# Kernel tuning notes

Hardware: AMD Instinct MI355X
Metric: run time of the kernel (lower is better)

Reference implementation:

```python
import jax, jax.numpy as jnp
import numpy as np

HEAD_NUM = 8
NEG = 10000.0


def setup_inputs() -> dict:
    key = jax.random.key(0)
    ks = jax.random.split(key, 8)
    B, S, D = 2, 2048, 512
    sc = 1.0 / np.sqrt(D)
    return {
        "x": jax.random.normal(ks[0], (B, S, D), dtype=jnp.float32),
        "mask": jax.random.randint(ks[1], (B, S), 0, 2, dtype=jnp.int32),
        "Wq": jax.random.normal(ks[2], (D, D), dtype=jnp.float32) * sc,
        "bq": jnp.zeros((D,), jnp.float32),
        "Wk": jax.random.normal(ks[3], (D, D), dtype=jnp.float32) * sc,
        "bk": jnp.zeros((D,), jnp.float32),
        "Wv": jax.random.normal(ks[4], (D, D), dtype=jnp.float32) * sc,
        "bv": jnp.zeros((D,), jnp.float32),
        "Wo": jax.random.normal(ks[5], (D, D), dtype=jnp.float32) * sc,
        "bo": jnp.zeros((D,), jnp.float32),
    }


def _split_heads(t, H):
    B, S, D = t.shape
    return t.reshape(B, S, H, D // H).transpose(0, 2, 1, 3)  # [B,H,S,hd]


def reference(x, mask, Wq, bq, Wk, bk, Wv, bv, Wo, bo):
    B, S, D = x.shape
    H = HEAD_NUM
    hd = D // H
    # linear projections + relu activation (as in keras layer)
    q = jax.nn.relu(x @ Wq + bq)
    k = jax.nn.relu(x @ Wk + bk)
    v = jax.nn.relu(x @ Wv + bv)
    q = _split_heads(q, H)
    k = _split_heads(k, H)
    v = _split_heads(v, H)
    # scaled dot-product scores: scale by sqrt(head_dim) (query last dim after split)
    e = jnp.einsum("bhqd,bhkd->bhqk", q, k) / jnp.sqrt(jnp.float32(hd))
    # causal (history_only) additive mask
    idx = jnp.arange(S)
    causal = (idx[None, :] > idx[:, None]).astype(jnp.float32)  # [S,S]
    e = e - NEG * causal[None, None, :, :]
    # key padding mask, additive
    e = e - NEG * (1.0 - mask.astype(jnp.float32))[:, None, None, :]
    # stable softmax (explicit max-subtract as in source)
    a = jax.nn.softmax(e, axis=-1)
    out = jnp.einsum("bhqk,bhkd->bhqd", a, v)  # [B,H,S,hd]
    out = out.transpose(0, 2, 1, 3).reshape(B, S, D)
    # output projection + activation
    return jax.nn.relu(out @ Wo + bo)
```

## Files before the change

### kernel.cpp

```cpp
#include <hip/hip_runtime.h>
#include <hip/hip_bf16.h>

constexpr int Bc = 2, Sc = 2048, Dc = 512, Hc = 8, HDc = 64;
constexpr int Mtot = Bc * Sc;
constexpr size_t HEADMAT = (size_t)Bc * Hc * Sc * HDc;
constexpr float SC2  = 0.18033688011112042f;
constexpr float NEG2 = 14426.950408889634f;

typedef __attribute__((ext_vector_type(8)))  short          short8;
typedef __attribute__((ext_vector_type(8)))  unsigned short ushort8;
typedef __attribute__((ext_vector_type(4)))  float          f32x4;
typedef __attribute__((ext_vector_type(16))) float          f32x16;

#define MFMA16 __builtin_amdgcn_mfma_f32_16x16x32_bf16
#define MFMA32 __builtin_amdgcn_mfma_f32_32x32x16_bf16

static __device__ __forceinline__ unsigned short f32_to_bf16_bits(float f) {
    unsigned int u = __builtin_bit_cast(unsigned int, f);
    unsigned int r = u + 0x7FFFu + ((u >> 16) & 1u);
    return (unsigned short)(r >> 16);
}
static __device__ __forceinline__ unsigned int pkbf(float a, float b) {
    return (unsigned int)f32_to_bf16_bits(a) |
           ((unsigned int)f32_to_bf16_bits(b) << 16);
}

__global__ __launch_bounds__(256)
void convert_x(const float* __restrict__ x, unsigned short* __restrict__ Xb, int n)
{
    const int i = (blockIdx.x * 256 + threadIdx.x) * 4;
    if (i >= n) return;
    const float4 v = *(const float4*)(x + i);
    ushort4 o;
    o.x = f32_to_bf16_bits(v.x);
    o.y = f32_to_bf16_bits(v.y);
    o.z = f32_to_bf16_bits(v.z);
    o.w = f32_to_bf16_bits(v.w);
    *(ushort4*)(Xb + i) = o;
}

__global__ __launch_bounds__(256)
void transpose_w(const float* __restrict__ W0, const float* __restrict__ W1,
                 const float* __restrict__ W2, const float* __restrict__ W3,
                 unsigned short* __restrict__ Wt)
{
    __shared__ float T[64][65];
    const int z = blockIdx.z;
    const float* Wp = (z == 0) ? W0 : (z == 1) ? W1 : (z == 2) ? W2 : W3;
    unsigned short* Op = Wt + (size_t)z * 512 * 512;

    const int kt = blockIdx.y * 64, nt = blockIdx.x * 64;
    const int t = threadIdx.x;
    const int r  = t >> 2, c4 = (t & 3) * 16;

    #pragma unroll
    for (int i = 0; i < 4; ++i) {
        const float4 v = *(const float4*)(Wp + (size_t)(kt + r) * 512 + nt + c4 + 4 * i);
        T[r][c4 + 4*i + 0] = v.x;
        T[r][c4 + 4*i + 1] = v.y;
        T[r][c4 + 4*i + 2] = v.z;
        T[r][c4 + 4*i + 3] = v.w;
    }
    __syncthreads();

    const int n = t >> 2, k4 = (t & 3) * 16;
    #pragma unroll
    for (int i = 0; i < 4; ++i) {
        ushort4 o;
        o.x = f32_to_bf16_bits(T[k4 + 4*i + 0][n]);
        o.y = f32_to_bf16_bits(T[k4 + 4*i + 1][n]);
        o.z = f32_to_bf16_bits(T[k4 + 4*i + 2][n]);
        o.w = f32_to_bf16_bits(T[k4 + 4*i + 3][n]);
        *(ushort4*)(Op + (size_t)(nt + n) * 512 + kt + k4 + 4 * i) = o;
    }
}

template<bool HEADOUT>
__global__ __launch_bounds__(256)
void gemm_tile(const unsigned short* __restrict__ Xb,
               const unsigned short* __restrict__ Wt,
               const float* __restrict__ b0, const float* __restrict__ b1,
               const float* __restrict__ b2,
               unsigned short* __restrict__ Hout,
               float* __restrict__ Yf)
{
    __shared__ short As[128 * 32];
    __shared__ short Bs[64 * 32];

    const int lane = threadIdx.x & 63, wave = threadIdx.x >> 6;
    const int c = lane & 15, g = lane >> 4;
    const int wr = wave >> 1, wc = wave & 1;
    const int z = blockIdx.z;
    const unsigned short* Wp = Wt + (size_t)z * 512 * 512;
    const float* bp = (z == 0) ? b0 : (z == 1) ? b1 : b2;
    const int bm = blockIdx.y * 128;
    const int bn = blockIdx.x * 64;

    const int srow = lane >> 2;
    const int scol = (lane & 3) * 8;

    f32x4 acc[4][2] = {};

    for (int k0 = 0; k0 < 512; k0 += 32) {
        __syncthreads();
        #pragma unroll
        for (int i = 0; i < 2; ++i) {
            const int row = (wave * 2 + i) * 16 + srow;
            const short8 v = *(const short8*)(Xb + (size_t)(bm + row) * 512 + k0 + scol);
            *(short8*)(&As[row * 32 + scol]) = v;
        }
        {
            const int row = wave * 16 + srow;
            const short8 v = *(const short8*)(Wp + (size_t)(bn + row) * 512 + k0 + scol);
            *(short8*)(&Bs[row * 32 + scol]) = v;
        }
        __syncthreads();

        short8 a[4], bfr[2];
        #pragma unroll
        for (int mi = 0; mi < 4; ++mi)
            a[mi] = *(const short8*)(&As[(wr * 64 + mi * 16 + c) * 32 + g * 8]);
        #pragma unroll
        for (int ni = 0; ni < 2; ++ni)
            bfr[ni] = *(const short8*)(&Bs[(wc * 32 + ni * 16 + c) * 32 + g * 8]);
        #pragma unroll
        for (int mi = 0; mi < 4; ++mi)
            #pragma unroll
            for (int ni = 0; ni < 2; ++ni)
                acc[mi][ni] = MFMA16(a[mi], bfr[ni], acc[mi][ni], 0, 0, 0);
    }

    #pragma unroll
    for (int mi = 0; mi < 4; ++mi) {
        #pragma unroll
        for (int ni = 0; ni < 2; ++ni) {
            const int n = bn + wc * 32 + ni * 16 + c;
            const float bias = bp[n];
            float v[4];
            #pragma unroll
            for (int r = 0; r < 4; ++r)
                v[r] = fmaxf(acc[mi][ni][r] + bias, 0.0f);
            const int mbase = bm + wr * 64 + mi * 16 + 4 * g;
            if constexpr (HEADOUT) {
                const int bb = mbase >> 11, ss = mbase & 2047;
                const int hh = n >> 6, hd = n & 63;
                if (z == 2) {
                    union { ushort4 u; unsigned short s[4]; } pk;
                    #pragma unroll
                    for (int r = 0; r < 4; ++r) pk.s[r] = f32_to_bf16_bits(v[r]);
                    *reinterpret_cast<ushort4*>(
                        Hout + (size_t)2 * HEADMAT +
                        ((size_t)(bb * Hc + hh) * HDc + hd) * Sc + ss) = pk.u;
                } else {
                    #pragma unroll
                    for (int r = 0; r < 4; ++r)
                        Hout[(size_t)z * HEADMAT +
                             (((size_t)(bb * Hc + hh) * Sc + ss + r) * HDc + hd)] =
                            f32_to_bf16_bits(v[r]);
                }
            } else {
                #pragma unroll
                for (int r = 0; r < 4; ++r)
                    Yf[(size_t)(mbase + r) * 512 + n] = v[r];
            }
        }
    }
}

__global__ __launch_bounds__(256)
void attn_mfma(const short* __restrict__ Qh, const short* __restrict__ Kh,
               const short* __restrict__ Vt, const int* __restrict__ mask,
               unsigned short* __restrict__ Ob)
{
    __shared__ __align__(16) char smem[4 * 8448 + 4 * 256];

    const int lane = threadIdx.x & 63;
    const int wave = threadIdx.x >> 6;
    const int bid  = blockIdx.x;
    const int swz  = (bid & 7) * 128 + (bid >> 3);
    const int t    = swz & 63;
    const int h    = (swz >> 6) & 7;
    const int b    = swz >> 9;
    const int q0   = t * 32;
    const int r32  = lane & 31;
    const int hi   = lane >> 5;

    char*  wreg = smem + wave * 8448;
    float* Lml  = (float*)(smem + 4 * 8448 + wave * 256);

    const size_t headoff = (size_t)(b * Hc + h) * Sc * HDc;
    const short* Qp = Qh + headoff;
    const short* Kp = Kh + headoff;
    const short* Vp = Vt + headoff;
    const int* mb = mask + b * Sc;

    int fb = Sc;
    for (int base = 0; base < Sc; base += 64) {
        unsigned long long bal = __ballot(mb[base + lane] != 0);
        if (bal) { fb = base + (__ffsll(bal) - 1); break; }
    }
    const int kmax = (fb <= q0) ? (q0 + 32) : Sc;
    const int kend = (kmax + 31) & ~31;
    const int nT   = kend >> 5;
    const int tpw  = (nT + 3) >> 2;
    const int kbeg = wave * tpw * 32;
    const int kfin = min(kend, kbeg + tpw * 32);

    short8 qf[4];
    #pragma unroll
    for (int j = 0; j < 4; ++j)
        qf[j] = *(const short8*)(Qp + (size_t)(q0 + r32) * HDc + j * 16 + hi * 8);

    f32x16 acc0 = {0,0,0,0,0,0,0,0,0,0,0,0,0,0,0,0};
    f32x16 acc1 = {0,0,0,0,0,0,0,0,0,0,0,0,0,0,0,0};
    float m = -1e30f, l = 0.0f;

    const short* vrow0 = Vp + (size_t)r32 * Sc + 8 * hi;
    const short* vrow1 = Vp + (size_t)(32 + r32) * Sc + 8 * hi;

    for (int k0 = kbeg; k0 < kfin; k0 += 32) {
        const short8 va0 = *(const short8*)(vrow0 + k0);
        const short8 va1 = *(const short8*)(vrow0 + k0 + 16);
        const short8 vb0 = *(const short8*)(vrow1 + k0);
        const short8 vb1 = *(const short8*)(vrow1 + k0 + 16);

        f32x16 s = {0,0,0,0,0,0,0,0,0,0,0,0,0,0,0,0};
        #pragma unroll
        for (int j = 0; j < 4; ++j) {
            const short8 kf =
                *(const short8*)(Kp + (size_t)(k0 + r32) * HDc + j * 16 + hi * 8);
            s = MFMA32(kf, qf[j], s, 0, 0, 0);
        }

        const unsigned long long bal = __ballot(mb[k0 + r32] != 0);
        const unsigned int mloc = ((unsigned int)bal) >> (4 * hi);

        float e[16];
        float tmax = -1e30f;
        if (k0 + 31 > q0) {
            #pragma unroll
            for (int r = 0; r < 16; ++r) {
                const int cr0 = (r & 3) + 8 * (r >> 2);
                float ev = s[r] * SC2;
                if (!((mloc >> cr0) & 1))            ev -= NEG2;
                if (k0 + cr0 + 4 * hi > q0 + r32)    ev -= NEG2;
                e[r] = ev;
                tmax = fmaxf(tmax, ev);
            }
        } else {
            #pragma unroll
            for (int r = 0; r < 16; ++r) {
                const int cr0 = (r & 3) + 8 * (r >> 2);
                float ev = s[r] * SC2;
                if (!((mloc >> cr0) & 1))            ev -= NEG2;
                e[r] = ev;
                tmax = fmaxf(tmax, ev);
            }
        }
        tmax = fmaxf(tmax, __shfl_xor(tmax, 32));

        if (__any(tmax > m)) {
            const float mn   = fmaxf(m, tmax);
            const float corr = __builtin_exp2f(m - mn);
            m = mn; l *= corr;
            acc0 *= corr;
            acc1 *= corr;
        }

        float ps = 0.f;
        #pragma unroll
        for (int r = 0; r < 16; ++r) {
            e[r] = __builtin_exp2f(e[r] - m);
            ps += e[r];
        }
        l += ps;

        const unsigned int A0 = pkbf(e[0],  e[1]),  B0 = pkbf(e[2],  e[3]);
        const unsigned int C0 = pkbf(e[4],  e[5]),  D0 = pkbf(e[6],  e[7]);
        const unsigned int A1 = pkbf(e[8],  e[9]),  B1 = pkbf(e[10], e[11]);
        const unsigned int C1 = pkbf(e[12], e[13]), D1 = pkbf(e[14], e[15]);
        const unsigned int A0s = (unsigned int)__shfl_xor((int)A0, 32);
        const unsigned int B0s = (unsigned int)__shfl_xor((int)B0, 32);
        const unsigned int C0s = (unsigned int)__shfl_xor((int)C0, 32);
        const unsigned int D0s = (unsigned int)__shfl_xor((int)D0, 32);
        const unsigned int A1s = (unsigned int)__shfl_xor((int)A1, 32);
        const unsigned int B1s = (unsigned int)__shfl_xor((int)B1, 32);
        const unsigned int C1s = (unsigned int)__shfl_xor((int)C1, 32);
        const unsigned int D1s = (unsigned int)__shfl_xor((int)D1, 32);

        union { unsigned int u[4]; short8 s8; } P0, P1;
        P0.u[0] = hi ? C0s : A0;  P0.u[1] = hi ? D0s : B0;
        P0.u[2] = hi ? C0  : A0s; P0.u[3] = hi ? D0  : B0s;
        P1.u[0] = hi ? C1s : A1;  P1.u[1] = hi ? D1s : B1;
        P1.u[2] = hi ? C1  : A1s; P1.u[3] = hi ? D1  : B1s;

        acc0 = MFMA32(va0, P0.s8, acc0, 0, 0, 0);
        acc0 = MFMA32(va1, P1.s8, acc0, 0, 0, 0);
        acc1 = MFMA32(vb0, P0.s8, acc1, 0, 0, 0);
        acc1 = MFMA32(vb1, P1.s8, acc1, 0, 0, 0);
    }

    l += __shfl_xor(l, 32);

    {
        float* Lacc = (float*)wreg;
        #pragma unroll
        for (int r = 0; r < 16; ++r) {
            Lacc[lane * 33 + r]      = acc0[r];
            Lacc[lane * 33 + 16 + r] = acc1[r];
        }
        if (lane < 32) { Lml[lane] = m; Lml[32 + lane] = l; }
    }
    __syncthreads();

    float mu[4], lu[4], M = -1e30f;
    #pragma unroll
    for (int u = 0; u < 4; ++u) {
        const float* LmlU = (const float*)(smem + 4 * 8448 + u * 256);
        mu[u] = LmlU[r32];
        lu[u] = LmlU[32 + r32];
        M = fmaxf(M, mu[u]);
    }
    float wgt[4], L = 0.f;
    #pragma unroll
    for (int u = 0; u < 4; ++u) {
        wgt[u] = __builtin_exp2f(mu[u] - M);
        L += wgt[u] * lu[u];
    }
    const float invL = 1.0f / L;

    #pragma unroll
    for (int jj = 0; jj < 8; ++jj) {
        const int j = wave * 8 + jj;
        float o = 0.f;
        #pragma unroll
        for (int u = 0; u < 4; ++u)
            o += wgt[u] * ((const float*)(smem + u * 8448))[lane * 33 + j];
        const int j16 = j & 15;
        const int d = (j16 & 3) + 8 * (j16 >> 2) + 4 * hi + 32 * (j >> 4);
        Ob[(size_t)(b * Sc + q0 + r32) * Dc + h * HDc + d] =
            f32_to_bf16_bits(o * invL);
    }
}

extern "C" void kernel_launch(void* const* d_in, const int* in_sizes, int n_in,
                              void* d_out, int out_size, void* d_ws, size_t ws_size,
                              hipStream_t stream) {
    const float* x  = (const float*)d_in[0];
    const int* mask = (const int*)d_in[1];
    const float* Wq = (const float*)d_in[2];
    const float* bq = (const float*)d_in[3];
    const float* Wk = (const float*)d_in[4];
    const float* bk = (const float*)d_in[5];
    const float* Wv = (const float*)d_in[6];
    const float* bv = (const float*)d_in[7];
    const float* Wo = (const float*)d_in[8];
    const float* bo = (const float*)d_in[9];
    float* out = (float*)d_out;

    unsigned short* Xb = (unsigned short*)d_ws;
    unsigned short* Wt = Xb + (size_t)Mtot * 512;
    unsigned short* Qh = Wt + (size_t)4 * 512 * 512;
    unsigned short* Kh = Qh + HEADMAT;
    unsigned short* Vt = Kh + HEADMAT;
    unsigned short* Ob = Vt + HEADMAT;

    convert_x<<<dim3((Mtot * 512) / 1024), dim3(256), 0, stream>>>(
        x, Xb, Mtot * 512);
    transpose_w<<<dim3(8, 8, 4), dim3(256), 0, stream>>>(Wq, Wk, Wv, Wo, Wt);
    gemm_tile<true><<<dim3(8, Mtot / 128, 3), dim3(256), 0, stream>>>(
        Xb, Wt, bq, bk, bv, Qh, nullptr);
    attn_mfma<<<dim3(1024), dim3(256), 0, stream>>>(
        (const short*)Qh, (const short*)Kh, (const short*)Vt, mask, Ob);
    gemm_tile<false><<<dim3(8, Mtot / 128, 1), dim3(256), 0, stream>>>(
        Ob, Wt + (size_t)3 * 512 * 512, bo, bo, bo, nullptr, out);
}
```

Measured before the change: 97.49 us.

## Split attention key range across eight waves and fold softmax scale into Q

Launches the attention kernel with 512 threads so eight waves each process a share of the key range, then merges partial accumulators in two rounds through the same shared-memory buffer. The softmax scale is folded into the Q projection epilogue, which removes a multiply per score. The bf16 packing now uses the HIP intrinsic, and the tile order is reversed so the long causal tiles launch first. Extra block barriers and the merge step add overhead, and scaling Q before bf16 rounding slightly changes the numerics.

```diff
diff --git a/kernel.cpp b/kernel.cpp
--- a/kernel.cpp
+++ b/kernel.cpp
@@ -20,9 +20,10 @@
     unsigned int r = u + 0x7FFFu + ((u >> 16) & 1u);
     return (unsigned short)(r >> 16);
 }
-static __device__ __forceinline__ unsigned int pkbf(float a, float b) {
-    return (unsigned int)f32_to_bf16_bits(a) |
-           ((unsigned int)f32_to_bf16_bits(b) << 16);
+static __device__ __forceinline__ unsigned int pk2bf(float a, float b) {
+    union { __hip_bfloat162 h2; unsigned int u; } cv;
+    cv.h2 = __float22bfloat162_rn(make_float2(a, b));
+    return cv.u;
 }
 
 __global__ __launch_bounds__(256)
@@ -138,8 +139,10 @@
             const float bias = bp[n];
             float v[4];
             #pragma unroll
-            for (int r = 0; r < 4; ++r)
+            for (int r = 0; r < 4; ++r) {
                 v[r] = fmaxf(acc[mi][ni][r] + bias, 0.0f);
+                if (HEADOUT && z == 0) v[r] *= SC2;
+            }
             const int mbase = bm + wr * 64 + mi * 16 + 4 * g;
             if constexpr (HEADOUT) {
                 const int bb = mbase >> 11, ss = mbase & 2047;
@@ -167,26 +170,25 @@
     }
 }
 
-__global__ __launch_bounds__(256)
+__global__ __launch_bounds__(512, 4)
 void attn_mfma(const short* __restrict__ Qh, const short* __restrict__ Kh,
                const short* __restrict__ Vt, const int* __restrict__ mask,
                unsigned short* __restrict__ Ob)
 {
-    __shared__ __align__(16) char smem[4 * 8448 + 4 * 256];
+    __shared__ __align__(16) char smem[4 * 8448 + 8 * 256];
 
     const int lane = threadIdx.x & 63;
     const int wave = threadIdx.x >> 6;
     const int bid  = blockIdx.x;
     const int swz  = (bid & 7) * 128 + (bid >> 3);
-    const int t    = swz & 63;
+    const int t    = 63 - (swz & 63);
     const int h    = (swz >> 6) & 7;
     const int b    = swz >> 9;
     const int q0   = t * 32;
     const int r32  = lane & 31;
     const int hi   = lane >> 5;
 
-    char*  wreg = smem + wave * 8448;
-    float* Lml  = (float*)(smem + 4 * 8448 + wave * 256);
+    float* Lml = (float*)(smem + 4 * 8448 + wave * 256);
 
     const size_t headoff = (size_t)(b * Hc + h) * Sc * HDc;
     const short* Qp = Qh + headoff;
@@ -202,7 +204,7 @@
     const int kmax = (fb <= q0) ? (q0 + 32) : Sc;
     const int kend = (kmax + 31) & ~31;
     const int nT   = kend >> 5;
-    const int tpw  = (nT + 3) >> 2;
+    const int tpw  = (nT + 7) >> 3;
     const int kbeg = wave * tpw * 32;
     const int kfin = min(kend, kbeg + tpw * 32);
 
@@ -241,7 +243,7 @@
             #pragma unroll
             for (int r = 0; r < 16; ++r) {
                 const int cr0 = (r & 3) + 8 * (r >> 2);
-                float ev = s[r] * SC2;
+                float ev = s[r];
                 if (!((mloc >> cr0) & 1))            ev -= NEG2;
                 if (k0 + cr0 + 4 * hi > q0 + r32)    ev -= NEG2;
                 e[r] = ev;
@@ -251,7 +253,7 @@
             #pragma unroll
             for (int r = 0; r < 16; ++r) {
                 const int cr0 = (r & 3) + 8 * (r >> 2);
-                float ev = s[r] * SC2;
+                float ev = s[r];
                 if (!((mloc >> cr0) & 1))            ev -= NEG2;
                 e[r] = ev;
                 tmax = fmaxf(tmax, ev);
@@ -275,10 +277,10 @@
         }
         l += ps;
 
-        const unsigned int A0 = pkbf(e[0],  e[1]),  B0 = pkbf(e[2],  e[3]);
-        const unsigned int C0 = pkbf(e[4],  e[5]),  D0 = pkbf(e[6],  e[7]);
-        const unsigned int A1 = pkbf(e[8],  e[9]),  B1 = pkbf(e[10], e[11]);
-        const unsigned int C1 = pkbf(e[12], e[13]), D1 = pkbf(e[14], e[15]);
+        const unsigned int A0 = pk2bf(e[0],  e[1]),  B0 = pk2bf(e[2],  e[3]);
+        const unsigned int C0 = pk2bf(e[4],  e[5]),  D0 = pk2bf(e[6],  e[7]);
+        const unsigned int A1 = pk2bf(e[8],  e[9]),  B1 = pk2bf(e[10], e[11]);
+        const unsigned int C1 = pk2bf(e[12], e[13]), D1 = pk2bf(e[14], e[15]);
         const unsigned int A0s = (unsigned int)__shfl_xor((int)A0, 32);
         const unsigned int B0s = (unsigned int)__shfl_xor((int)B0, 32);
         const unsigned int C0s = (unsigned int)__shfl_xor((int)C0, 32);
@@ -302,44 +304,65 @@
 
     l += __shfl_xor(l, 32);
 
-    {
-        float* Lacc = (float*)wreg;
-        #pragma unroll
-        for (int r = 0; r < 16; ++r) {
-            Lacc[lane * 33 + r]      = acc0[r];
-            Lacc[lane * 33 + 16 + r] = acc1[r];
-        }
-        if (lane < 32) { Lml[lane] = m; Lml[32 + lane] = l; }
-    }
+    if (lane < 32) { Lml[lane] = m; Lml[32 + lane] = l; }
     __syncthreads();
 
-    float mu[4], lu[4], M = -1e30f;
-    #pragma unroll
-    for (int u = 0; u < 4; ++u) {
+    float mu[8], lu[8], M = -1e30f;
+    #pragma unroll
+    for (int u = 0; u < 8; ++u) {
         const float* LmlU = (const float*)(smem + 4 * 8448 + u * 256);
         mu[u] = LmlU[r32];
         lu[u] = LmlU[32 + r32];
         M = fmaxf(M, mu[u]);
     }
-    float wgt[4], L = 0.f;
-    #pragma unroll
-    for (int u = 0; u < 4; ++u) {
+    float wgt[8], L = 0.f;
+    #pragma unroll
+    for (int u = 0; u < 8; ++u) {
         wgt[u] = __builtin_exp2f(mu[u] - M);
         L += wgt[u] * lu[u];
     }
     const float invL = 1.0f / L;
 
-    #pragma unroll
-    for (int jj = 0; jj < 8; ++jj) {
-        const int j = wave * 8 + jj;
-        float o = 0.f;
+    if (wave < 4) {
+        float* Lacc = (float*)(smem + wave * 8448);
+        #pragma unroll
+        for (int r = 0; r < 16; ++r) {
+            Lacc[lane * 33 + r]      = acc0[r];
+            Lacc[lane * 33 + 16 + r] = acc1[r];
+        }
+    }
+    __syncthreads();
+    float o[4];
+    #pragma unroll
+    for (int jj = 0; jj < 4; ++jj) {
+        const int j = wave * 4 + jj;
+        float v = 0.f;
         #pragma unroll
         for (int u = 0; u < 4; ++u)
-            o += wgt[u] * ((const float*)(smem + u * 8448))[lane * 33 + j];
+            v += wgt[u] * ((const float*)(smem + u * 8448))[lane * 33 + j];
+        o[jj] = v;
+    }
+    __syncthreads();
+    if (wave >= 4) {
+        float* Lacc = (float*)(smem + (wave - 4) * 8448);
+        #pragma unroll
+        for (int r = 0; r < 16; ++r) {
+            Lacc[lane * 33 + r]      = acc0[r];
+            Lacc[lane * 33 + 16 + r] = acc1[r];
+        }
+    }
+    __syncthreads();
+    #pragma unroll
+    for (int jj = 0; jj < 4; ++jj) {
+        const int j = wave * 4 + jj;
+        float v = o[jj];
+        #pragma unroll
+        for (int u = 4; u < 8; ++u)
+            v += wgt[u] * ((const float*)(smem + (u - 4) * 8448))[lane * 33 + j];
         const int j16 = j & 15;
         const int d = (j16 & 3) + 8 * (j16 >> 2) + 4 * hi + 32 * (j >> 4);
         Ob[(size_t)(b * Sc + q0 + r32) * Dc + h * HDc + d] =
-            f32_to_bf16_bits(o * invL);
+            f32_to_bf16_bits(v * invL);
     }
 }
 
@@ -370,7 +393,7 @@
     transpose_w<<<dim3(8, 8, 4), dim3(256), 0, stream>>>(Wq, Wk, Wv, Wo, Wt);
     gemm_tile<true><<<dim3(8, Mtot / 128, 3), dim3(256), 0, stream>>>(
         Xb, Wt, bq, bk, bv, Qh, nullptr);
-    attn_mfma<<<dim3(1024), dim3(256), 0, stream>>>(
+    attn_mfma<<<dim3(1024), dim3(512), 0, stream>>>(
         (const short*)Qh, (const short*)Kh, (const short*)Vt, mask, Ob);
     gemm_tile<false><<<dim3(8, Mtot / 128, 1), dim3(256), 0, stream>>>(
         Ob, Wt + (size_t)3 * 512 * 512, bo, bo, bo, nullptr, out);
```

Result: slower. 117.2 us (+20.2%).
